# Optimization experiments

Measured on AMD Instinct MI355X. Metric: run time of the kernel, lower is better.

The kernel has to match this reference:

```python
import jax, jax.numpy as jnp
import numpy as np

BN_EPS = 1e-5


def _conv(x, w, stride, pad):
    return jax.lax.conv_general_dilated(
        x, w, (stride, stride), [(pad, pad), (pad, pad)],
        dimension_numbers=('NCHW', 'OIHW', 'NCHW'))


def setup_inputs() -> dict:
    key = jax.random.key(0)
    ks = jax.random.split(key, 6)
    b, c, h, w = 8, 32, 80, 160
    guidance = jax.random.normal(ks[0], (b, c, 2 * h, 2 * w), dtype=jnp.float32)
    # positive disparities, realistic magnitude
    disp = jax.random.uniform(ks[1], (b, 1, h, w), dtype=jnp.float32) * 24.0
    conv1_w = jax.random.normal(ks[2], (2 * c, c, 3, 3), dtype=jnp.float32) * 0.05
    bn_gamma = jnp.ones((2 * c,), dtype=jnp.float32)
    bn_beta = jnp.zeros((2 * c,), dtype=jnp.float32)
    bn_mean = jax.random.normal(ks[3], (2 * c,), dtype=jnp.float32) * 0.1
    bn_var = jax.random.uniform(ks[4], (2 * c,), dtype=jnp.float32, minval=0.5, maxval=1.5)
    conv2_w = jax.random.normal(ks[5], (9 * 64, 2 * c, 3, 3), dtype=jnp.float32) * 0.05
    return {'guidance': guidance, 'disp': disp, 'conv1_w': conv1_w,
            'bn_gamma': bn_gamma, 'bn_beta': bn_beta, 'bn_mean': bn_mean,
            'bn_var': bn_var, 'conv2_w': conv2_w}


def reference(guidance, disp, conv1_w, bn_gamma, bn_beta, bn_mean, bn_var, conv2_w):
    b, _, h, w = disp.shape
    # mask branch: convbn(stride 2) + ReLU + conv -> 9*64 channels at (h, w)
    x = _conv(guidance, conv1_w, 2, 1)
    inv = jax.lax.rsqrt(bn_var + BN_EPS)
    x = (x - bn_mean[None, :, None, None]) * (inv * bn_gamma)[None, :, None, None] + bn_beta[None, :, None, None]
    x = jax.nn.relu(x)
    mask = _conv(x, conv2_w, 1, 1).reshape(b, 1, 9, 8, 8, h, w)
    mask = jax.nn.softmax(mask, axis=2)
    # unfold(8*disp, 3x3, pad=1) -> (b, 1, 9, h, w), row-major kernel order
    d8 = jnp.pad(8.0 * disp, ((0, 0), (0, 0), (1, 1), (1, 1)))
    patches = jnp.stack([d8[:, :, i:i + h, j:j + w]
                         for i in range(3) for j in range(3)], axis=2)
    # convex combination over the 9 neighbors
    up = jnp.sum(mask * patches[:, :, :, None, None], axis=2)  # (b,1,8,8,h,w)
    up = up.transpose(0, 1, 4, 2, 5, 3)  # (b,1,h,8,w,8)
    return up.reshape(b, 1, 8 * h, 8 * w)
```

## Files before the change

kernel.cpp:

```cpp
#include <hip/hip_runtime.h>
#include <math.h>

typedef _Float16 half8 __attribute__((ext_vector_type(8)));
typedef float f32x4 __attribute__((ext_vector_type(4)));

constexpr int B_ = 8;
constexpr int HG = 160, WG = 320;
constexpr int H = 80, W = 160;
constexpr size_t CWS_OFF  = 0;
constexpr size_t W1WS_OFF = 663552;
constexpr size_t XG_OFF   = 700416;

__global__ __launch_bounds__(256) void prep(const float* __restrict__ w1,
                                            const float* __restrict__ w2,
                                            char* __restrict__ ws)
{
    int e = blockIdx.x * 256 + threadIdx.x;
    if (e < 576 * 64) {
        int n = e >> 6, cin = e & 63;
        int k = n >> 6, ng = (n >> 4) & 3, nl = n & 15;
        int kl = cin & 31, c5 = cin >> 5;
        const float* src = w2 + ((size_t)(n * 64 + cin)) * 9;
        int fragoff = ((kl >> 3) * 16 + nl) * 16 + (kl & 7) * 2;
#pragma unroll
        for (int t = 0; t < 9; ++t) {
            int s = t * 2 + c5;
            *(_Float16*)(ws + CWS_OFF + (size_t)ng * 165888
                         + (size_t)(s * 9 + k) * 1024 + fragoff) = (_Float16)src[t];
        }
    } else if (e < 576 * 64 + 64 * 32) {
        int e2 = e - 576 * 64;
        int ch = e2 >> 5, cin = e2 & 31;
        const float* src = w1 + ((size_t)(ch * 32 + cin)) * 9;
        int fragoff = (ch >> 4) * 1024 + ((cin >> 3) * 16 + (ch & 15)) * 16 + (cin & 7) * 2;
#pragma unroll
        for (int t = 0; t < 9; ++t)
            *(_Float16*)(ws + W1WS_OFF + (size_t)t * 4096 + fragoff) = (_Float16)src[t];
    }
}

__global__ __launch_bounds__(256, 4) void conv1_mfma(
    const float* __restrict__ g, const char* __restrict__ ws_w1,
    const float* __restrict__ gamma, const float* __restrict__ beta,
    const float* __restrict__ mean, const float* __restrict__ var,
    _Float16* __restrict__ xg)
{
    const int tx0 = blockIdx.x * 16, ty0 = blockIdx.y * 8, b = blockIdx.z;
    __shared__ __align__(16) _Float16 gl[2][17][18][32];
    const int tid = threadIdx.x;

    const int gy0 = 2 * ty0 - 1;
    const int gxa0 = 2 * tx0 - 2;
    for (int i = tid; i < 17 * 32 * 17; i += 256) {
        int wr = i / 544; int rem = i - wr * 544;
        int cin = rem / 17; int c2 = rem - cin * 17;
        int gy = gy0 + wr;
        int gxa = gxa0 + 2 * c2;
        float2 v = make_float2(0.f, 0.f);
        if (gy >= 0 && gy < HG && gxa >= 0)
            v = *(const float2*)(g + ((size_t)(b * 32 + cin) * HG + gy) * WG + gxa);
        int slot = cin >> 3, elem = cin & 7;
        if (c2 > 0) {
            int wch = c2 - 1;
            gl[1][wr][wch][((slot ^ ((wch >> 1) & 3)) << 3) + elem] = (_Float16)v.x;
        }
        {
            int wch = c2;
            gl[0][wr][wch][((slot ^ ((wch >> 1) & 3)) << 3) + elem] = (_Float16)v.y;
        }
    }

    const int lane = tid & 63, w = tid >> 6;
    const int c = lane & 15, grp = lane >> 4;

    const _Float16* w1p = (const _Float16*)ws_w1 + lane * 8;
    half8 bf[4];
#pragma unroll
    for (int nt = 0; nt < 4; ++nt) bf[nt] = *(const half8*)(w1p + nt * 512);

    f32x4 zf = {0.f, 0.f, 0.f, 0.f};
    f32x4 acc[2][4];
#pragma unroll
    for (int mt = 0; mt < 2; ++mt)
#pragma unroll
        for (int nt = 0; nt < 4; ++nt) acc[mt][nt] = zf;

    __syncthreads();

#pragma unroll
    for (int s = 0; s < 9; ++s) {
        const int dy = s / 3, dx = s - dy * 3;
        const int par = dx & 1, dxh = dx >> 1;
        half8 af[2];
#pragma unroll
        for (int mt = 0; mt < 2; ++mt) {
            int wr = 2 * (2 * w + mt) + dy;
            int wch = c + dxh;
            af[mt] = *(const half8*)&gl[par][wr][wch][(grp ^ ((wch >> 1) & 3)) << 3];
        }
        const _Float16* wnext = w1p + (size_t)(s + 1) * 2048;
#pragma unroll
        for (int nt = 0; nt < 4; ++nt) {
            half8 cur = bf[nt];
            bf[nt] = *(const half8*)(wnext + nt * 512);
            acc[0][nt] = __builtin_amdgcn_mfma_f32_16x16x32_f16(af[0], cur, acc[0][nt], 0, 0, 0);
            acc[1][nt] = __builtin_amdgcn_mfma_f32_16x16x32_f16(af[1], cur, acc[1][nt], 0, 0, 0);
        }
    }

#pragma unroll
    for (int nt = 0; nt < 4; ++nt) {
        int ch = nt * 16 + c;
        float mu = mean[ch], scv = rsqrtf(var[ch] + 1e-5f) * gamma[ch], bt = beta[ch];
#pragma unroll
        for (int mt = 0; mt < 2; ++mt) {
            int y = ty0 + 2 * w + mt;
#pragma unroll
            for (int r = 0; r < 4; ++r) {
                int x = tx0 + grp * 4 + r;
                float v = fmaxf((acc[mt][nt][r] - mu) * scv + bt, 0.f);
                xg[(((size_t)(b * H + y) * W + x) << 6) + ch] = (_Float16)v;
            }
        }
    }
}

__global__ __launch_bounds__(512, 2) void conv2_mfma(
    const _Float16* __restrict__ xg, const char* __restrict__ ws_c,
    const float* __restrict__ disp, float* __restrict__ out)
{
    const int tx0 = blockIdx.x * 16, ty0 = blockIdx.y * 8, b = blockIdx.z;
    __shared__ __align__(16) _Float16 xs[180 * 64];
    __shared__ float d8s[180];
    const int tid = threadIdx.x;
    const int lane = tid & 63, wid = tid >> 6;

    half8 zero8;
#pragma unroll
    for (int j = 0; j < 8; ++j) zero8[j] = (_Float16)0.f;
    for (int cidx = tid; cidx < 1440; cidx += 512) {
        int wp = cidx >> 3, slot = cidx & 7;
        int rr = wp / 18, cc = wp - rr * 18;
        int y = ty0 - 1 + rr, xc = tx0 - 1 + cc;
        half8 v = zero8;
        if (y >= 0 && y < H && xc >= 0 && xc < W)
            v = *(const half8*)(xg + (((size_t)(b * H + y) * W + xc) << 6) + slot * 8);
        *(half8*)&xs[wp * 64 + (slot ^ (wp & 7)) * 8] = v;
    }
    if (tid < 180) {
        int rr = tid / 18, cc = tid - rr * 18;
        int y = ty0 - 1 + rr, xc = tx0 - 1 + cc;
        float v = 0.f;
        if (y >= 0 && y < H && xc >= 0 && xc < W) v = 8.f * disp[(b * H + y) * W + xc];
        d8s[tid] = v;
    }

    const int ng = wid & 3, mg = wid >> 2;
    const int c = lane & 15, grp = lane >> 4;

    f32x4 zf = {0.f, 0.f, 0.f, 0.f};
    f32x4 acc[4][9];
#pragma unroll
    for (int m = 0; m < 4; ++m)
#pragma unroll
        for (int k = 0; k < 9; ++k) acc[m][k] = zf;

    const _Float16* wp = (const _Float16*)ws_c + (size_t)ng * 82944 + lane * 8;

    half8 bf[9];
#pragma unroll
    for (int k = 0; k < 9; ++k) bf[k] = *(const half8*)(wp + k * 512);

    __syncthreads();

#pragma unroll 2
    for (int s = 0; s < 18; ++s) {
        const int t = s >> 1;
        const int dy = t / 3, dx = t - dy * 3;
        const int aslot = (s & 1) * 4 + grp;
        half8 af[4];
#pragma unroll
        for (int mt = 0; mt < 4; ++mt) {
            int wrow = (mg * 4 + mt + dy) * 18 + c + dx;
            af[mt] = *(const half8*)&xs[wrow * 64 + (aslot ^ (wrow & 7)) * 8];
        }
        const _Float16* wnext = wp + (size_t)(s + 1) * 4608;
#pragma unroll
        for (int k = 0; k < 9; ++k) {
            half8 cur = bf[k];
            bf[k] = *(const half8*)(wnext + k * 512);
#pragma unroll
            for (int mt = 0; mt < 4; ++mt)
                acc[mt][k] = __builtin_amdgcn_mfma_f32_16x16x32_f16(
                    af[mt], cur, acc[mt][k], 0, 0, 0);
        }
    }

    const int ij = ng * 16 + c;
    const int oi = ij >> 3, oj = ij & 7;
#pragma unroll
    for (int mt = 0; mt < 4; ++mt) {
#pragma unroll
        for (int r = 0; r < 4; ++r) {
            int pr = mg * 4 + mt, pc = grp * 4 + r;
            float pat[9];
#pragma unroll
            for (int k9 = 0; k9 < 9; ++k9) pat[k9] = d8s[(pr + k9 / 3) * 18 + pc + k9 % 3];
            float mx = acc[mt][0][r];
#pragma unroll
            for (int k9 = 1; k9 < 9; ++k9) mx = fmaxf(mx, acc[mt][k9][r]);
            float sum = 0.f, up = 0.f;
#pragma unroll
            for (int k9 = 0; k9 < 9; ++k9) {
                float e = __expf(acc[mt][k9][r] - mx);
                sum += e; up += e * pat[k9];
            }
            int y = ty0 + pr, xc = tx0 + pc;
            out[((size_t)(b * (8 * H) + y * 8 + oi)) * (size_t)(8 * W) + xc * 8 + oj] = up / sum;
        }
    }
}

extern "C" void kernel_launch(void* const* d_in, const int* in_sizes, int n_in,
                              void* d_out, int out_size, void* d_ws, size_t ws_size,
                              hipStream_t stream)
{
    const float* guidance = (const float*)d_in[0];
    const float* disp     = (const float*)d_in[1];
    const float* conv1_w  = (const float*)d_in[2];
    const float* bn_gamma = (const float*)d_in[3];
    const float* bn_beta  = (const float*)d_in[4];
    const float* bn_mean  = (const float*)d_in[5];
    const float* bn_var   = (const float*)d_in[6];
    const float* conv2_w  = (const float*)d_in[7];
    float* out = (float*)d_out;
    char* ws = (char*)d_ws;
    _Float16* xg = (_Float16*)(ws + XG_OFF);

    prep<<<dim3((576 * 64 + 64 * 32 + 255) / 256), dim3(256), 0, stream>>>(
        conv1_w, conv2_w, ws);
    dim3 grid1(W / 16, H / 8, B_);
    conv1_mfma<<<grid1, dim3(256), 0, stream>>>(
        guidance, ws + W1WS_OFF, bn_gamma, bn_beta, bn_mean, bn_var, xg);
    dim3 grid2(W / 16, H / 8, B_);
    conv2_mfma<<<grid2, dim3(512), 0, stream>>>(
        xg, ws + CWS_OFF, disp, out);
}
```

Baseline: 120.1 us.

## Make conv2 a persistent kernel with atomic tile scheduling and smaller tiles

The conv2+softmax-upsample kernel becomes a persistent grid of 1024 blocks of 256 threads. Each block pulls 4x16-pixel tiles from a global atomic counter, which is zeroed by a memset before launch. Each wave now covers one 16-channel output group over the whole 4-row tile, instead of splitting rows across wave pairs. The aim is better load balance and occupancy across CUs. The cost is more halo reloading per tile, repeated weight fetches for every tile, and an atomic plus extra barriers per tile.

```diff
diff --git a/kernel.cpp b/kernel.cpp
--- a/kernel.cpp
+++ b/kernel.cpp
@@ -10,6 +10,7 @@
 constexpr size_t CWS_OFF  = 0;
 constexpr size_t W1WS_OFF = 663552;
 constexpr size_t XG_OFF   = 700416;
+constexpr size_t CNT_OFF  = 13807616;
 
 __global__ __launch_bounds__(256) void prep(const float* __restrict__ w1,
                                             const float* __restrict__ w2,
@@ -125,98 +126,109 @@
     }
 }
 
-__global__ __launch_bounds__(512, 2) void conv2_mfma(
+__global__ __launch_bounds__(256, 2) void conv2_mfma(
     const _Float16* __restrict__ xg, const char* __restrict__ ws_c,
-    const float* __restrict__ disp, float* __restrict__ out)
-{
-    const int tx0 = blockIdx.x * 16, ty0 = blockIdx.y * 8, b = blockIdx.z;
-    __shared__ __align__(16) _Float16 xs[180 * 64];
-    __shared__ float d8s[180];
+    const float* __restrict__ disp, float* __restrict__ out,
+    int* __restrict__ cnt)
+{
+    __shared__ __align__(16) _Float16 xs[108 * 64];
+    __shared__ float d8s[108];
+    __shared__ int s_tile;
     const int tid = threadIdx.x;
     const int lane = tid & 63, wid = tid >> 6;
+    const int c = lane & 15, grp = lane >> 4;
+
+    const _Float16* wp = (const _Float16*)ws_c + (size_t)wid * 82944 + lane * 8;
 
     half8 zero8;
 #pragma unroll
     for (int j = 0; j < 8; ++j) zero8[j] = (_Float16)0.f;
-    for (int cidx = tid; cidx < 1440; cidx += 512) {
-        int wp = cidx >> 3, slot = cidx & 7;
-        int rr = wp / 18, cc = wp - rr * 18;
-        int y = ty0 - 1 + rr, xc = tx0 - 1 + cc;
-        half8 v = zero8;
-        if (y >= 0 && y < H && xc >= 0 && xc < W)
-            v = *(const half8*)(xg + (((size_t)(b * H + y) * W + xc) << 6) + slot * 8);
-        *(half8*)&xs[wp * 64 + (slot ^ (wp & 7)) * 8] = v;
-    }
-    if (tid < 180) {
-        int rr = tid / 18, cc = tid - rr * 18;
-        int y = ty0 - 1 + rr, xc = tx0 - 1 + cc;
-        float v = 0.f;
-        if (y >= 0 && y < H && xc >= 0 && xc < W) v = 8.f * disp[(b * H + y) * W + xc];
-        d8s[tid] = v;
-    }
-
-    const int ng = wid & 3, mg = wid >> 2;
-    const int c = lane & 15, grp = lane >> 4;
-
-    f32x4 zf = {0.f, 0.f, 0.f, 0.f};
-    f32x4 acc[4][9];
-#pragma unroll
-    for (int m = 0; m < 4; ++m)
-#pragma unroll
-        for (int k = 0; k < 9; ++k) acc[m][k] = zf;
-
-    const _Float16* wp = (const _Float16*)ws_c + (size_t)ng * 82944 + lane * 8;
-
-    half8 bf[9];
-#pragma unroll
-    for (int k = 0; k < 9; ++k) bf[k] = *(const half8*)(wp + k * 512);
-
-    __syncthreads();
+
+    for (;;) {
+        if (tid == 0) s_tile = atomicAdd(cnt, 1);
+        __syncthreads();
+        const int tile = __builtin_amdgcn_readfirstlane(s_tile);
+        if (tile >= 1600) break;
+        const int b   = tile / 200;
+        const int rem = tile - b * 200;
+        const int tyi = rem / 10;
+        const int tx0 = (rem - tyi * 10) * 16, ty0 = tyi * 4;
+
+        for (int cidx = tid; cidx < 864; cidx += 256) {
+            int wpx = cidx >> 3, slot = cidx & 7;
+            int rr = wpx / 18, cc = wpx - rr * 18;
+            int y = ty0 - 1 + rr, xc = tx0 - 1 + cc;
+            half8 v = zero8;
+            if (y >= 0 && y < H && xc >= 0 && xc < W)
+                v = *(const half8*)(xg + (((size_t)(b * H + y) * W + xc) << 6) + slot * 8);
+            *(half8*)&xs[wpx * 64 + (slot ^ (wpx & 7)) * 8] = v;
+        }
+        if (tid < 108) {
+            int rr = tid / 18, cc = tid - rr * 18;
+            int y = ty0 - 1 + rr, xc = tx0 - 1 + cc;
+            float v = 0.f;
+            if (y >= 0 && y < H && xc >= 0 && xc < W) v = 8.f * disp[(b * H + y) * W + xc];
+            d8s[tid] = v;
+        }
+
+        f32x4 zf = {0.f, 0.f, 0.f, 0.f};
+        f32x4 acc[4][9];
+#pragma unroll
+        for (int m = 0; m < 4; ++m)
+#pragma unroll
+            for (int k = 0; k < 9; ++k) acc[m][k] = zf;
+
+        half8 bf[9];
+#pragma unroll
+        for (int k = 0; k < 9; ++k) bf[k] = *(const half8*)(wp + k * 512);
+
+        __syncthreads();
 
 #pragma unroll 2
-    for (int s = 0; s < 18; ++s) {
-        const int t = s >> 1;
-        const int dy = t / 3, dx = t - dy * 3;
-        const int aslot = (s & 1) * 4 + grp;
-        half8 af[4];
+        for (int s = 0; s < 18; ++s) {
+            const int t = s >> 1;
+            const int dy = t / 3, dx = t - dy * 3;
+            const int aslot = (s & 1) * 4 + grp;
+            half8 af[4];
+#pragma unroll
+            for (int mt = 0; mt < 4; ++mt) {
+                int wrow = (mt + dy) * 18 + c + dx;
+                af[mt] = *(const half8*)&xs[wrow * 64 + (aslot ^ (wrow & 7)) * 8];
+            }
+            const _Float16* wnext = wp + (size_t)(s + 1) * 4608;
+#pragma unroll
+            for (int k = 0; k < 9; ++k) {
+                half8 cur = bf[k];
+                bf[k] = *(const half8*)(wnext + k * 512);
+#pragma unroll
+                for (int mt = 0; mt < 4; ++mt)
+                    acc[mt][k] = __builtin_amdgcn_mfma_f32_16x16x32_f16(
+                        af[mt], cur, acc[mt][k], 0, 0, 0);
+            }
+        }
+
+        const int ij = wid * 16 + c;
+        const int oi = ij >> 3, oj = ij & 7;
 #pragma unroll
         for (int mt = 0; mt < 4; ++mt) {
-            int wrow = (mg * 4 + mt + dy) * 18 + c + dx;
-            af[mt] = *(const half8*)&xs[wrow * 64 + (aslot ^ (wrow & 7)) * 8];
-        }
-        const _Float16* wnext = wp + (size_t)(s + 1) * 4608;
-#pragma unroll
-        for (int k = 0; k < 9; ++k) {
-            half8 cur = bf[k];
-            bf[k] = *(const half8*)(wnext + k * 512);
-#pragma unroll
-            for (int mt = 0; mt < 4; ++mt)
-                acc[mt][k] = __builtin_amdgcn_mfma_f32_16x16x32_f16(
-                    af[mt], cur, acc[mt][k], 0, 0, 0);
-        }
-    }
-
-    const int ij = ng * 16 + c;
-    const int oi = ij >> 3, oj = ij & 7;
-#pragma unroll
-    for (int mt = 0; mt < 4; ++mt) {
-#pragma unroll
-        for (int r = 0; r < 4; ++r) {
-            int pr = mg * 4 + mt, pc = grp * 4 + r;
-            float pat[9];
-#pragma unroll
-            for (int k9 = 0; k9 < 9; ++k9) pat[k9] = d8s[(pr + k9 / 3) * 18 + pc + k9 % 3];
-            float mx = acc[mt][0][r];
-#pragma unroll
-            for (int k9 = 1; k9 < 9; ++k9) mx = fmaxf(mx, acc[mt][k9][r]);
-            float sum = 0.f, up = 0.f;
-#pragma unroll
-            for (int k9 = 0; k9 < 9; ++k9) {
-                float e = __expf(acc[mt][k9][r] - mx);
-                sum += e; up += e * pat[k9];
-            }
-            int y = ty0 + pr, xc = tx0 + pc;
-            out[((size_t)(b * (8 * H) + y * 8 + oi)) * (size_t)(8 * W) + xc * 8 + oj] = up / sum;
+#pragma unroll
+            for (int r = 0; r < 4; ++r) {
+                int pr = mt, pc = grp * 4 + r;
+                float pat[9];
+#pragma unroll
+                for (int k9 = 0; k9 < 9; ++k9) pat[k9] = d8s[(pr + k9 / 3) * 18 + pc + k9 % 3];
+                float mx = acc[mt][0][r];
+#pragma unroll
+                for (int k9 = 1; k9 < 9; ++k9) mx = fmaxf(mx, acc[mt][k9][r]);
+                float sum = 0.f, up = 0.f;
+#pragma unroll
+                for (int k9 = 0; k9 < 9; ++k9) {
+                    float e = __expf(acc[mt][k9][r] - mx);
+                    sum += e; up += e * pat[k9];
+                }
+                int y = ty0 + pr, xc = tx0 + pc;
+                out[((size_t)(b * (8 * H) + y * 8 + oi)) * (size_t)(8 * W) + xc * 8 + oj] = up / sum;
+            }
         }
     }
 }
@@ -236,13 +248,14 @@
     float* out = (float*)d_out;
     char* ws = (char*)d_ws;
     _Float16* xg = (_Float16*)(ws + XG_OFF);
-
+    int* cnt = (int*)(ws + CNT_OFF);
+
+    hipMemsetAsync(cnt, 0, sizeof(int), stream);
     prep<<<dim3((576 * 64 + 64 * 32 + 255) / 256), dim3(256), 0, stream>>>(
         conv1_w, conv2_w, ws);
     dim3 grid1(W / 16, H / 8, B_);
     conv1_mfma<<<grid1, dim3(256), 0, stream>>>(
         guidance, ws + W1WS_OFF, bn_gamma, bn_beta, bn_mean, bn_var, xg);
-    dim3 grid2(W / 16, H / 8, B_);
-    conv2_mfma<<<grid2, dim3(512), 0, stream>>>(
-        xg, ws + CWS_OFF, disp, out);
-}
+    conv2_mfma<<<dim3(1024), dim3(256), 0, stream>>>(
+        xg, ws + CWS_OFF, disp, out, cnt);
+}
```

After: 124.2 us. 3.4% more time.
